# Optimization experiments

Hardware: AMD Instinct MI355X
Metric: run time of the kernel (lower is better)

## Reference

```python
import jax, jax.numpy as jnp
import numpy as np

N, E = 50000, 800000
IN_DIM, HID, OUT_DIM = 512, 64, 40


def setup_inputs() -> dict:
    key = jax.random.key(0)
    ks = jax.random.split(key, 7)
    X = jax.random.normal(ks[0], (N, IN_DIM), dtype=jnp.float32)
    edges = jax.random.randint(ks[1], (2, E), 0, N, dtype=jnp.int64)
    # GCNConv weight (glorot) and bias
    W1 = jax.random.normal(ks[2], (IN_DIM, HID), dtype=jnp.float32) / np.sqrt(IN_DIM)
    b1 = jnp.zeros((HID,), dtype=jnp.float32)
    # fc Linear
    Wfc = jax.random.normal(ks[3], (OUT_DIM, HID), dtype=jnp.float32) / np.sqrt(HID)
    bfc = jax.random.normal(ks[4], (OUT_DIM,), dtype=jnp.float32) * 0.01
    return {"X": X, "edges": edges, "W1": W1, "b1": b1, "Wfc": Wfc, "bfc": bfc}


def gcn_conv(x, src, dst, W, b, n):
    # PyG GCNConv: transform, add self-loops, symmetric D^-1/2 A D^-1/2 norm,
    # scatter-add messages at destination, add bias.
    h = x @ W  # [N, HID]
    loop = jnp.arange(n, dtype=src.dtype)
    src = jnp.concatenate([src, loop])
    dst = jnp.concatenate([dst, loop])
    deg = jax.ops.segment_sum(jnp.ones_like(dst, dtype=h.dtype), dst, num_segments=n)
    dinv = jnp.where(deg > 0, jax.lax.rsqrt(deg), 0.0)
    coef = dinv[src] * dinv[dst]  # [E+N]
    msgs = coef[:, None] * h[src]  # gather + scale
    agg = jax.ops.segment_sum(msgs, dst, num_segments=n)  # scatter-add
    return agg + b


def reference(X, edges, W1, b1, Wfc, bfc):
    n = X.shape[0]
    src, dst = edges[0], edges[1]
    h = jax.nn.relu(gcn_conv(X, src, dst, W1, b1, n))  # [N, HID]
    return h @ Wfc.T + bfc  # [N, OUT_DIM]
```

## Files before the change

kernel.cpp:

```cpp
#include <hip/hip_runtime.h>
#include <hip/hip_bf16.h>

typedef unsigned short u16;
typedef __bf16 bf16_8 __attribute__((ext_vector_type(8)));
typedef float f32_4 __attribute__((ext_vector_type(4)));

#define IN_DIM 512
#define HID 64
#define OUT_DIM 40
#define CAP 64
#define CF_BLOCKS 512

__global__ void k_prep(const float* __restrict__ W1, u16* __restrict__ W1t,
                       int* __restrict__ cnt, int n) {
    int i = blockIdx.x * 256 + threadIdx.x;
    if (i < n) cnt[i] = 0;
    if (i < IN_DIM * HID) {
        int k = i / HID, o = i % HID;
        __hip_bfloat16 v = __float2bfloat16(W1[i]);
        W1t[o * IN_DIM + k] = *reinterpret_cast<u16*>(&v);
    }
}

__launch_bounds__(256)
__global__ void k_work(const float* __restrict__ X, const u16* __restrict__ W1t,
                       const int* __restrict__ src, const int* __restrict__ dst,
                       int* cnt, u16* __restrict__ csr, u16* __restrict__ hs,
                       int N, int E, int NT) {
    __shared__ __align__(16) u16 As[2][64 * 40];
    const int t = threadIdx.x;

    if ((int)blockIdx.x >= NT) {
        int tid = ((int)blockIdx.x - NT) * 256 + t;
        int stride = CF_BLOCKS * 256;
        for (int e = tid; e < E; e += stride) {
            int d = dst[e];
            int p = atomicAdd(&cnt[d], 1);
            if (p < CAP) csr[(size_t)d * CAP + p] = (u16)src[e];
        }
        return;
    }

    const int wave = t >> 6;
    const int lane = t & 63;
    const int m = lane & 15;
    const int quad = lane >> 4;
    const int n0 = blockIdx.x * 64;

    f32_4 acc[4];
    #pragma unroll
    for (int c = 0; c < 4; c++) acc[c] = (f32_4){0.f, 0.f, 0.f, 0.f};

    const int r_st = t >> 2;
    const int k_st = (t & 3) * 8;

    int row = n0 + r_st; if (row >= N) row = N - 1;
    const float* xp = X + (size_t)row * IN_DIM + k_st;

    f32_4 x0 = *reinterpret_cast<const f32_4*>(xp);
    f32_4 x1 = *reinterpret_cast<const f32_4*>(xp + 4);

    int buf = 0;
    for (int k0 = 0; k0 < IN_DIM; k0 += 32) {
        u16 xb[8];
        #pragma unroll
        for (int q = 0; q < 4; q++) {
            __hip_bfloat16 c0 = __float2bfloat16(x0[q]);
            __hip_bfloat16 c1 = __float2bfloat16(x1[q]);
            xb[q]     = *reinterpret_cast<u16*>(&c0);
            xb[4 + q] = *reinterpret_cast<u16*>(&c1);
        }
        *reinterpret_cast<uint4*>(&As[buf][r_st * 40 + k_st]) = *reinterpret_cast<uint4*>(xb);
        __syncthreads();

        if (k0 + 32 < IN_DIM) {
            x0 = *reinterpret_cast<const f32_4*>(xp + k0 + 32);
            x1 = *reinterpret_cast<const f32_4*>(xp + k0 + 36);
        }

        bf16_8 a = *reinterpret_cast<const bf16_8*>(&As[buf][(wave * 16 + m) * 40 + quad * 8]);
        #pragma unroll
        for (int c = 0; c < 4; c++) {
            bf16_8 b = *reinterpret_cast<const bf16_8*>(
                W1t + (size_t)(c * 16 + m) * IN_DIM + k0 + quad * 8);
            acc[c] = __builtin_amdgcn_mfma_f32_16x16x32_bf16(a, b, acc[c], 0, 0, 0);
        }
        buf ^= 1;
    }

    const int nbase = n0 + wave * 16 + quad * 4;
    #pragma unroll
    for (int r = 0; r < 4; r++) {
        int n = nbase + r;
        if (n < N) {
            #pragma unroll
            for (int c = 0; c < 4; c++) {
                __hip_bfloat16 hv = __float2bfloat16(acc[c][r]);
                hs[(size_t)n * HID + c * 16 + m] = *reinterpret_cast<u16*>(&hv);
            }
        }
    }
}

__device__ __forceinline__ void cvt_accs(f32_4& a, uint2 v, float s) {
    a[0] += s * __uint_as_float(v.x << 16);
    a[1] += s * __uint_as_float(v.x & 0xFFFF0000u);
    a[2] += s * __uint_as_float(v.y << 16);
    a[3] += s * __uint_as_float(v.y & 0xFFFF0000u);
}

#define SHP 72

__launch_bounds__(256)
__global__ void k_aggfc(const u16* __restrict__ hs, const u16* __restrict__ csr,
                        const int* __restrict__ cnt, const float* __restrict__ b1,
                        const float* __restrict__ Wfc, const float* __restrict__ bfc,
                        float* __restrict__ out, int N) {
    __shared__ __align__(16) u16 shb[16 * SHP];
    __shared__ __align__(16) u16 wfb[48 * SHP];
    __shared__ float bl[48];
    const int t = threadIdx.x;

    for (int i = t; i < 48 * HID; i += 256) {
        int o = i / HID, k = i % HID;
        float v = (o < OUT_DIM) ? Wfc[o * HID + k] : 0.f;
        __hip_bfloat16 b = __float2bfloat16(v);
        wfb[o * SHP + k] = *reinterpret_cast<u16*>(&b);
    }
    if (t < 48) bl[t] = (t < OUT_DIM) ? bfc[t] : 0.f;

    const int g = t >> 4, l = t & 15;
    const int n = blockIdx.x * 16 + g;

    if (n < N) {
        const uint2* hs2 = reinterpret_cast<const uint2*>(hs);
        f32_4 a0 = (f32_4){0.f, 0.f, 0.f, 0.f};
        f32_4 a1 = a0, a2 = a0, a3 = a0;
        const float dvn = rsqrtf((float)cnt[n] + 1.0f);
        cvt_accs(a0, hs2[(size_t)n * 16 + l], dvn);
        int deg = cnt[n]; if (deg > CAP) deg = CAP;
        const u16* cs = csr + (size_t)n * CAP;
        int j = 0;
        for (; j + 7 < deg; j += 8) {
            int s0 = cs[j],     s1 = cs[j + 1], s2 = cs[j + 2], s3 = cs[j + 3];
            int s4 = cs[j + 4], s5 = cs[j + 5], s6 = cs[j + 6], s7 = cs[j + 7];
            float d0 = rsqrtf((float)cnt[s0] + 1.0f);
            float d1 = rsqrtf((float)cnt[s1] + 1.0f);
            float d2 = rsqrtf((float)cnt[s2] + 1.0f);
            float d3 = rsqrtf((float)cnt[s3] + 1.0f);
            float d4 = rsqrtf((float)cnt[s4] + 1.0f);
            float d5 = rsqrtf((float)cnt[s5] + 1.0f);
            float d6 = rsqrtf((float)cnt[s6] + 1.0f);
            float d7 = rsqrtf((float)cnt[s7] + 1.0f);
            uint2 v0 = hs2[(size_t)s0 * 16 + l];
            uint2 v1 = hs2[(size_t)s1 * 16 + l];
            uint2 v2 = hs2[(size_t)s2 * 16 + l];
            uint2 v3 = hs2[(size_t)s3 * 16 + l];
            uint2 v4 = hs2[(size_t)s4 * 16 + l];
            uint2 v5 = hs2[(size_t)s5 * 16 + l];
            uint2 v6 = hs2[(size_t)s6 * 16 + l];
            uint2 v7 = hs2[(size_t)s7 * 16 + l];
            cvt_accs(a0, v0, d0); cvt_accs(a1, v1, d1);
            cvt_accs(a2, v2, d2); cvt_accs(a3, v3, d3);
            cvt_accs(a0, v4, d4); cvt_accs(a1, v5, d5);
            cvt_accs(a2, v6, d6); cvt_accs(a3, v7, d7);
        }
        for (; j < deg; j++) {
            int s = cs[j];
            cvt_accs(a0, hs2[(size_t)s * 16 + l], rsqrtf((float)cnt[s] + 1.0f));
        }
        f32_4 acc = (a0 + a1) + (a2 + a3);
        u16 rb[4];
        #pragma unroll
        for (int q = 0; q < 4; q++) {
            float x = dvn * acc[q] + b1[l * 4 + q];
            x = x > 0.f ? x : 0.f;
            __hip_bfloat16 hb = __float2bfloat16(x);
            rb[q] = *reinterpret_cast<u16*>(&hb);
        }
        *reinterpret_cast<uint2*>(&shb[g * SHP + l * 4]) = *reinterpret_cast<uint2*>(rb);
    }
    __syncthreads();

    const int wave = t >> 6;
    const int lane = t & 63;
    const int m = lane & 15;
    const int quad = lane >> 4;
    if (wave < 3) {
        bf16_8 a0 = *reinterpret_cast<const bf16_8*>(&shb[m * SHP + quad * 8]);
        bf16_8 a1 = *reinterpret_cast<const bf16_8*>(&shb[m * SHP + 32 + quad * 8]);
        bf16_8 b0 = *reinterpret_cast<const bf16_8*>(&wfb[(wave * 16 + m) * SHP + quad * 8]);
        bf16_8 b1 = *reinterpret_cast<const bf16_8*>(&wfb[(wave * 16 + m) * SHP + 32 + quad * 8]);
        f32_4 c = (f32_4){0.f, 0.f, 0.f, 0.f};
        c = __builtin_amdgcn_mfma_f32_16x16x32_bf16(a0, b0, c, 0, 0, 0);
        c = __builtin_amdgcn_mfma_f32_16x16x32_bf16(a1, b1, c, 0, 0, 0);
        const int o = wave * 16 + m;
        if (o < OUT_DIM) {
            const int base = blockIdx.x * 16;
            #pragma unroll
            for (int r = 0; r < 4; r++) {
                int node = base + quad * 4 + r;
                if (node < N) out[(size_t)node * OUT_DIM + o] = c[r] + bl[o];
            }
        }
    }
}


extern "C" void kernel_launch(void* const* d_in, const int* in_sizes, int n_in,
                              void* d_out, int out_size, void* d_ws, size_t ws_size,
                              hipStream_t stream) {
    const float* X   = (const float*)d_in[0];
    const int* edges = (const int*)d_in[1];
    const float* W1  = (const float*)d_in[2];
    const float* b1  = (const float*)d_in[3];
    const float* Wfc = (const float*)d_in[4];
    const float* bfc = (const float*)d_in[5];

    const int N = in_sizes[0] / IN_DIM;
    const int E = in_sizes[1] / 2;
    const int* src = edges;
    const int* dst = edges + E;

    char* p = (char*)d_ws;
    auto carve = [&](size_t bytes) -> char* {
        char* r = p;
        p += (bytes + 255) & ~(size_t)255;
        return r;
    };
    u16* W1t = (u16*)carve((size_t)IN_DIM * HID * 2);
    u16* hs  = (u16*)carve((size_t)N * HID * 2);
    int* cnt = (int*)carve((size_t)N * 4);
    u16* csr = (u16*)carve((size_t)N * CAP * 2);

    const int nb = (N + 255) / 256;
    const int NT = (N + 63) / 64;

    k_prep <<<nb, 256, 0, stream>>>(W1, W1t, cnt, N);
    k_work <<<NT + CF_BLOCKS, 256, 0, stream>>>(X, W1t, src, dst, cnt, csr, hs, N, E, NT);
    k_aggfc<<<(N + 15) / 16, 256, 0, stream>>>(hs, csr, cnt, b1, Wfc, bfc,
                                               (float*)d_out, N);
}
```

Measured before the change: 236.1 us.

## Pre-scale features by source degree norm and load CSR row via shuffles

Adds a k_scale pass that multiplies each node's bf16 features by its D^-1/2 factor. This removes the per-edge random cnt lookups and rsqrt calls in aggregation, and the CSR row is now loaded once per lane and broadcast with shuffles. The GEMM part of k_work drops the LDS staging and __syncthreads and loads X directly into MFMA operands, with the k-loop fully unrolled. The edge-count blocks are moved to the front of the grid, raised to 768 and unrolled by four. The new pass adds an extra read/write of hs, and rounding the scaled features to bf16 changes numerics slightly.

```diff
diff --git a/kernel.cpp b/kernel.cpp
--- a/kernel.cpp
+++ b/kernel.cpp
@@ -9,7 +9,7 @@
 #define HID 64
 #define OUT_DIM 40
 #define CAP 64
-#define CF_BLOCKS 512
+#define CF_BLOCKS 768
 
 __global__ void k_prep(const float* __restrict__ W1, u16* __restrict__ W1t,
                        int* __restrict__ cnt, int n) {
@@ -26,14 +26,32 @@
 __global__ void k_work(const float* __restrict__ X, const u16* __restrict__ W1t,
                        const int* __restrict__ src, const int* __restrict__ dst,
                        int* cnt, u16* __restrict__ csr, u16* __restrict__ hs,
-                       int N, int E, int NT) {
-    __shared__ __align__(16) u16 As[2][64 * 40];
+                       int N, int E) {
     const int t = threadIdx.x;
 
-    if ((int)blockIdx.x >= NT) {
-        int tid = ((int)blockIdx.x - NT) * 256 + t;
-        int stride = CF_BLOCKS * 256;
-        for (int e = tid; e < E; e += stride) {
+    if ((int)blockIdx.x < CF_BLOCKS) {
+        int tid = (int)blockIdx.x * 256 + t;
+        const int stride = CF_BLOCKS * 256;
+        int e = tid;
+        for (; e + 3 * stride < E; e += 4 * stride) {
+            int d0 = dst[e];
+            int d1 = dst[e + stride];
+            int d2 = dst[e + 2 * stride];
+            int d3 = dst[e + 3 * stride];
+            int s0 = src[e];
+            int s1 = src[e + stride];
+            int s2 = src[e + 2 * stride];
+            int s3 = src[e + 3 * stride];
+            int p0 = atomicAdd(&cnt[d0], 1);
+            int p1 = atomicAdd(&cnt[d1], 1);
+            int p2 = atomicAdd(&cnt[d2], 1);
+            int p3 = atomicAdd(&cnt[d3], 1);
+            if (p0 < CAP) csr[(size_t)d0 * CAP + p0] = (u16)s0;
+            if (p1 < CAP) csr[(size_t)d1 * CAP + p1] = (u16)s1;
+            if (p2 < CAP) csr[(size_t)d2 * CAP + p2] = (u16)s2;
+            if (p3 < CAP) csr[(size_t)d3 * CAP + p3] = (u16)s3;
+        }
+        for (; e < E; e += stride) {
             int d = dst[e];
             int p = atomicAdd(&cnt[d], 1);
             if (p < CAP) csr[(size_t)d * CAP + p] = (u16)src[e];
@@ -41,51 +59,39 @@
         return;
     }
 
+    const int tile = (int)blockIdx.x - CF_BLOCKS;
     const int wave = t >> 6;
     const int lane = t & 63;
     const int m = lane & 15;
     const int quad = lane >> 4;
-    const int n0 = blockIdx.x * 64;
+    const int n0 = tile * 64;
+
+    int row = n0 + wave * 16 + m;
+    if (row >= N) row = N - 1;
+    const float* xp = X + (size_t)row * IN_DIM + quad * 8;
+    const u16* bp = W1t + (size_t)m * IN_DIM + quad * 8;
 
     f32_4 acc[4];
     #pragma unroll
     for (int c = 0; c < 4; c++) acc[c] = (f32_4){0.f, 0.f, 0.f, 0.f};
 
-    const int r_st = t >> 2;
-    const int k_st = (t & 3) * 8;
-
-    int row = n0 + r_st; if (row >= N) row = N - 1;
-    const float* xp = X + (size_t)row * IN_DIM + k_st;
-
-    f32_4 x0 = *reinterpret_cast<const f32_4*>(xp);
-    f32_4 x1 = *reinterpret_cast<const f32_4*>(xp + 4);
-
-    int buf = 0;
+    #pragma unroll
     for (int k0 = 0; k0 < IN_DIM; k0 += 32) {
-        u16 xb[8];
+        f32_4 x0 = *reinterpret_cast<const f32_4*>(xp + k0);
+        f32_4 x1 = *reinterpret_cast<const f32_4*>(xp + k0 + 4);
+        union { bf16_8 v; u16 s[8]; } au;
         #pragma unroll
         for (int q = 0; q < 4; q++) {
             __hip_bfloat16 c0 = __float2bfloat16(x0[q]);
             __hip_bfloat16 c1 = __float2bfloat16(x1[q]);
-            xb[q]     = *reinterpret_cast<u16*>(&c0);
-            xb[4 + q] = *reinterpret_cast<u16*>(&c1);
-        }
-        *reinterpret_cast<uint4*>(&As[buf][r_st * 40 + k_st]) = *reinterpret_cast<uint4*>(xb);
-        __syncthreads();
-
-        if (k0 + 32 < IN_DIM) {
-            x0 = *reinterpret_cast<const f32_4*>(xp + k0 + 32);
-            x1 = *reinterpret_cast<const f32_4*>(xp + k0 + 36);
-        }
-
-        bf16_8 a = *reinterpret_cast<const bf16_8*>(&As[buf][(wave * 16 + m) * 40 + quad * 8]);
+            au.s[q]     = *reinterpret_cast<u16*>(&c0);
+            au.s[4 + q] = *reinterpret_cast<u16*>(&c1);
+        }
         #pragma unroll
         for (int c = 0; c < 4; c++) {
-            bf16_8 b = *reinterpret_cast<const bf16_8*>(
-                W1t + (size_t)(c * 16 + m) * IN_DIM + k0 + quad * 8);
-            acc[c] = __builtin_amdgcn_mfma_f32_16x16x32_bf16(a, b, acc[c], 0, 0, 0);
-        }
-        buf ^= 1;
+            bf16_8 b = *reinterpret_cast<const bf16_8*>(bp + (size_t)c * 16 * IN_DIM + k0);
+            acc[c] = __builtin_amdgcn_mfma_f32_16x16x32_bf16(au.v, b, acc[c], 0, 0, 0);
+        }
     }
 
     const int nbase = n0 + wave * 16 + quad * 4;
@@ -102,11 +108,31 @@
     }
 }
 
-__device__ __forceinline__ void cvt_accs(f32_4& a, uint2 v, float s) {
-    a[0] += s * __uint_as_float(v.x << 16);
-    a[1] += s * __uint_as_float(v.x & 0xFFFF0000u);
-    a[2] += s * __uint_as_float(v.y << 16);
-    a[3] += s * __uint_as_float(v.y & 0xFFFF0000u);
+__global__ void k_scale(u16* __restrict__ hs, const int* __restrict__ cnt, int N) {
+    int i = blockIdx.x * 256 + threadIdx.x;
+    int node = i >> 3;
+    if (node >= N) return;
+    float dv = rsqrtf((float)cnt[node] + 1.0f);
+    uint4 v = *reinterpret_cast<uint4*>(hs + (size_t)i * 8);
+    uint vv[4] = {v.x, v.y, v.z, v.w};
+    u16 o[8];
+    #pragma unroll
+    for (int q = 0; q < 4; q++) {
+        float lo = __uint_as_float(vv[q] << 16) * dv;
+        float hi = __uint_as_float(vv[q] & 0xFFFF0000u) * dv;
+        __hip_bfloat16 bl_ = __float2bfloat16(lo);
+        __hip_bfloat16 bh_ = __float2bfloat16(hi);
+        o[2 * q]     = *reinterpret_cast<u16*>(&bl_);
+        o[2 * q + 1] = *reinterpret_cast<u16*>(&bh_);
+    }
+    *reinterpret_cast<uint4*>(hs + (size_t)i * 8) = *reinterpret_cast<uint4*>(o);
+}
+
+__device__ __forceinline__ void acc_add(f32_4& a, uint2 v) {
+    a[0] += __uint_as_float(v.x << 16);
+    a[1] += __uint_as_float(v.x & 0xFFFF0000u);
+    a[2] += __uint_as_float(v.y << 16);
+    a[3] += __uint_as_float(v.y & 0xFFFF0000u);
 }
 
 #define SHP 72
@@ -137,21 +163,20 @@
         f32_4 a0 = (f32_4){0.f, 0.f, 0.f, 0.f};
         f32_4 a1 = a0, a2 = a0, a3 = a0;
         const float dvn = rsqrtf((float)cnt[n] + 1.0f);
-        cvt_accs(a0, hs2[(size_t)n * 16 + l], dvn);
+        acc_add(a0, hs2[(size_t)n * 16 + l]);
         int deg = cnt[n]; if (deg > CAP) deg = CAP;
-        const u16* cs = csr + (size_t)n * CAP;
+        uint2 cv = reinterpret_cast<const uint2*>(csr + (size_t)n * CAP)[l];
         int j = 0;
         for (; j + 7 < deg; j += 8) {
-            int s0 = cs[j],     s1 = cs[j + 1], s2 = cs[j + 2], s3 = cs[j + 3];
-            int s4 = cs[j + 4], s5 = cs[j + 5], s6 = cs[j + 6], s7 = cs[j + 7];
-            float d0 = rsqrtf((float)cnt[s0] + 1.0f);
-            float d1 = rsqrtf((float)cnt[s1] + 1.0f);
-            float d2 = rsqrtf((float)cnt[s2] + 1.0f);
-            float d3 = rsqrtf((float)cnt[s3] + 1.0f);
-            float d4 = rsqrtf((float)cnt[s4] + 1.0f);
-            float d5 = rsqrtf((float)cnt[s5] + 1.0f);
-            float d6 = rsqrtf((float)cnt[s6] + 1.0f);
-            float d7 = rsqrtf((float)cnt[s7] + 1.0f);
+            int base = j >> 2;
+            uint w0x = __shfl(cv.x, base, 16);
+            uint w0y = __shfl(cv.y, base, 16);
+            uint w1x = __shfl(cv.x, base + 1, 16);
+            uint w1y = __shfl(cv.y, base + 1, 16);
+            int s0 = (int)(w0x & 0xffff), s1 = (int)(w0x >> 16);
+            int s2 = (int)(w0y & 0xffff), s3 = (int)(w0y >> 16);
+            int s4 = (int)(w1x & 0xffff), s5 = (int)(w1x >> 16);
+            int s6 = (int)(w1y & 0xffff), s7 = (int)(w1y >> 16);
             uint2 v0 = hs2[(size_t)s0 * 16 + l];
             uint2 v1 = hs2[(size_t)s1 * 16 + l];
             uint2 v2 = hs2[(size_t)s2 * 16 + l];
@@ -160,14 +185,15 @@
             uint2 v5 = hs2[(size_t)s5 * 16 + l];
             uint2 v6 = hs2[(size_t)s6 * 16 + l];
             uint2 v7 = hs2[(size_t)s7 * 16 + l];
-            cvt_accs(a0, v0, d0); cvt_accs(a1, v1, d1);
-            cvt_accs(a2, v2, d2); cvt_accs(a3, v3, d3);
-            cvt_accs(a0, v4, d4); cvt_accs(a1, v5, d5);
-            cvt_accs(a2, v6, d6); cvt_accs(a3, v7, d7);
+            acc_add(a0, v0); acc_add(a1, v1);
+            acc_add(a2, v2); acc_add(a3, v3);
+            acc_add(a0, v4); acc_add(a1, v5);
+            acc_add(a2, v6); acc_add(a3, v7);
         }
         for (; j < deg; j++) {
-            int s = cs[j];
-            cvt_accs(a0, hs2[(size_t)s * 16 + l], rsqrtf((float)cnt[s] + 1.0f));
+            uint w = __shfl(((j >> 1) & 1) ? cv.y : cv.x, j >> 2, 16);
+            int s = (int)((w >> ((j & 1) * 16)) & 0xffff);
+            acc_add(a0, hs2[(size_t)s * 16 + l]);
         }
         f32_4 acc = (a0 + a1) + (a2 + a3);
         u16 rb[4];
@@ -237,7 +263,8 @@
     const int NT = (N + 63) / 64;
 
     k_prep <<<nb, 256, 0, stream>>>(W1, W1t, cnt, N);
-    k_work <<<NT + CF_BLOCKS, 256, 0, stream>>>(X, W1t, src, dst, cnt, csr, hs, N, E, NT);
+    k_work <<<CF_BLOCKS + NT, 256, 0, stream>>>(X, W1t, src, dst, cnt, csr, hs, N, E);
+    k_scale<<<(N * 8 + 255) / 256, 256, 0, stream>>>(hs, cnt, N);
     k_aggfc<<<(N + 15) / 16, 256, 0, stream>>>(hs, csr, cnt, b1, Wfc, bfc,
                                                (float*)d_out, N);
 }
```

New measurement: 262.5 us. +11.2%, slower.

## Prescale hidden features by inverse degree and shuffle-broadcast CSR neighbor indices

Applied to the files above, without the earlier changes.

Adds a small kernel that multiplies each node's bf16 hidden row by its D^-1/2 factor once. This removes the per-edge dependent gather of the source degree and its rsqrt from the aggregation loop. The aggregation kernel now loads each node's CSR row once as a vector per 16-lane group and hands neighbor indices to the lanes with width-16 shuffles, replacing repeated scalar index loads. In exchange there is an extra launch, an extra read/write pass over the hidden buffer, and a second bf16 rounding of the scaled values.

```diff
diff --git a/kernel.cpp b/kernel.cpp
--- a/kernel.cpp
+++ b/kernel.cpp
@@ -102,11 +102,31 @@
     }
 }
 
-__device__ __forceinline__ void cvt_accs(f32_4& a, uint2 v, float s) {
-    a[0] += s * __uint_as_float(v.x << 16);
-    a[1] += s * __uint_as_float(v.x & 0xFFFF0000u);
-    a[2] += s * __uint_as_float(v.y << 16);
-    a[3] += s * __uint_as_float(v.y & 0xFFFF0000u);
+__global__ void k_scale(u16* __restrict__ hs, const int* __restrict__ cnt, int N) {
+    int i = blockIdx.x * 256 + threadIdx.x;
+    int node = i >> 3;
+    if (node >= N) return;
+    float dv = rsqrtf((float)cnt[node] + 1.0f);
+    uint4 v = *reinterpret_cast<uint4*>(hs + (size_t)i * 8);
+    uint vv[4] = {v.x, v.y, v.z, v.w};
+    u16 o[8];
+    #pragma unroll
+    for (int q = 0; q < 4; q++) {
+        float lo = __uint_as_float(vv[q] << 16) * dv;
+        float hi = __uint_as_float(vv[q] & 0xFFFF0000u) * dv;
+        __hip_bfloat16 bl_ = __float2bfloat16(lo);
+        __hip_bfloat16 bh_ = __float2bfloat16(hi);
+        o[2 * q]     = *reinterpret_cast<u16*>(&bl_);
+        o[2 * q + 1] = *reinterpret_cast<u16*>(&bh_);
+    }
+    *reinterpret_cast<uint4*>(hs + (size_t)i * 8) = *reinterpret_cast<uint4*>(o);
+}
+
+__device__ __forceinline__ void acc_add(f32_4& a, uint2 v) {
+    a[0] += __uint_as_float(v.x << 16);
+    a[1] += __uint_as_float(v.x & 0xFFFF0000u);
+    a[2] += __uint_as_float(v.y << 16);
+    a[3] += __uint_as_float(v.y & 0xFFFF0000u);
 }
 
 #define SHP 72
@@ -137,21 +157,20 @@
         f32_4 a0 = (f32_4){0.f, 0.f, 0.f, 0.f};
         f32_4 a1 = a0, a2 = a0, a3 = a0;
         const float dvn = rsqrtf((float)cnt[n] + 1.0f);
-        cvt_accs(a0, hs2[(size_t)n * 16 + l], dvn);
+        acc_add(a0, hs2[(size_t)n * 16 + l]);
         int deg = cnt[n]; if (deg > CAP) deg = CAP;
-        const u16* cs = csr + (size_t)n * CAP;
+        uint2 cv = reinterpret_cast<const uint2*>(csr + (size_t)n * CAP)[l];
         int j = 0;
         for (; j + 7 < deg; j += 8) {
-            int s0 = cs[j],     s1 = cs[j + 1], s2 = cs[j + 2], s3 = cs[j + 3];
-            int s4 = cs[j + 4], s5 = cs[j + 5], s6 = cs[j + 6], s7 = cs[j + 7];
-            float d0 = rsqrtf((float)cnt[s0] + 1.0f);
-            float d1 = rsqrtf((float)cnt[s1] + 1.0f);
-            float d2 = rsqrtf((float)cnt[s2] + 1.0f);
-            float d3 = rsqrtf((float)cnt[s3] + 1.0f);
-            float d4 = rsqrtf((float)cnt[s4] + 1.0f);
-            float d5 = rsqrtf((float)cnt[s5] + 1.0f);
-            float d6 = rsqrtf((float)cnt[s6] + 1.0f);
-            float d7 = rsqrtf((float)cnt[s7] + 1.0f);
+            int base = j >> 2;
+            uint w0x = __shfl(cv.x, base, 16);
+            uint w0y = __shfl(cv.y, base, 16);
+            uint w1x = __shfl(cv.x, base + 1, 16);
+            uint w1y = __shfl(cv.y, base + 1, 16);
+            int s0 = (int)(w0x & 0xffff), s1 = (int)(w0x >> 16);
+            int s2 = (int)(w0y & 0xffff), s3 = (int)(w0y >> 16);
+            int s4 = (int)(w1x & 0xffff), s5 = (int)(w1x >> 16);
+            int s6 = (int)(w1y & 0xffff), s7 = (int)(w1y >> 16);
             uint2 v0 = hs2[(size_t)s0 * 16 + l];
             uint2 v1 = hs2[(size_t)s1 * 16 + l];
             uint2 v2 = hs2[(size_t)s2 * 16 + l];
@@ -160,14 +179,15 @@
             uint2 v5 = hs2[(size_t)s5 * 16 + l];
             uint2 v6 = hs2[(size_t)s6 * 16 + l];
             uint2 v7 = hs2[(size_t)s7 * 16 + l];
-            cvt_accs(a0, v0, d0); cvt_accs(a1, v1, d1);
-            cvt_accs(a2, v2, d2); cvt_accs(a3, v3, d3);
-            cvt_accs(a0, v4, d4); cvt_accs(a1, v5, d5);
-            cvt_accs(a2, v6, d6); cvt_accs(a3, v7, d7);
+            acc_add(a0, v0); acc_add(a1, v1);
+            acc_add(a2, v2); acc_add(a3, v3);
+            acc_add(a0, v4); acc_add(a1, v5);
+            acc_add(a2, v6); acc_add(a3, v7);
         }
         for (; j < deg; j++) {
-            int s = cs[j];
-            cvt_accs(a0, hs2[(size_t)s * 16 + l], rsqrtf((float)cnt[s] + 1.0f));
+            uint w = __shfl(((j >> 1) & 1) ? cv.y : cv.x, j >> 2, 16);
+            int s = (int)((w >> ((j & 1) * 16)) & 0xffff);
+            acc_add(a0, hs2[(size_t)s * 16 + l]);
         }
         f32_4 acc = (a0 + a1) + (a2 + a3);
         u16 rb[4];
@@ -238,6 +258,7 @@
 
     k_prep <<<nb, 256, 0, stream>>>(W1, W1t, cnt, N);
     k_work <<<NT + CF_BLOCKS, 256, 0, stream>>>(X, W1t, src, dst, cnt, csr, hs, N, E, NT);
+    k_scale<<<(N * 8 + 255) / 256, 256, 0, stream>>>(hs, cnt, N);
     k_aggfc<<<(N + 15) / 16, 256, 0, stream>>>(hs, csr, cnt, b1, Wfc, bfc,
                                                (float*)d_out, N);
 }
```

Measured after the change: 232.1 us. No clear change (-1.7%).
